# Performance work log

Measured on AMD Instinct MI355X. Metric: run time of the kernel, lower is better.

The kernel has to match this reference:

```python
import jax, jax.numpy as jnp
import numpy as np
import math

H, C = 16, 4


def _clustering(x, alv, mu, log_var, log_prior, mi_estimation):
    # x: [B,h,L,D], alv: [B,h,L], mu/log_var: [h or 1, C, D], log_prior: [h or 1, C]
    B, Hh, L, D = x.shape
    z = x  # eval mode: no reparameterization noise
    zd = z[:, :, :, None, :]                       # [B,h,L,1,D]
    mu_b = mu[:, None, :, :]                       # [h,1,C,D]
    lv = log_var[:, None, :, :]
    var = jnp.exp(lv)
    lp = jax.nn.log_softmax(log_prior, axis=-1)    # [h,C]
    mse = (zd - mu_b) ** 2 / var                   # [B,h,L,C,D]
    log_pdf = -0.5 * mse.sum(-1) - 0.5 * lv.sum(-1) - D * math.pi  # [B,h,L,C]
    log_pdf = log_pdf + lp[:, None, :]
    shift = jax.lax.stop_gradient(log_pdf.max(axis=-1, keepdims=True))
    log_probs = jax.nn.log_softmax(log_pdf - shift + 5.0, axis=-1)
    cp = jnp.exp(log_probs)                        # cluster probs [B,h,L,C]
    lp_b = jnp.broadcast_to(lp[None, :, None, :], log_probs.shape)
    # F.kl_div(log_probs, prior) = prior * (log prior - log_probs)
    kl = (jnp.exp(lp_b) * (lp_b - log_probs)).sum(-1).mean(axis=(1, 2))
    alv5 = alv[:, :, :, None, None]
    avar = jnp.exp(alv5)
    kl = kl + 0.5 * (cp * (mse + avar / var + lv).sum(-1)).sum(-1).mean(axis=(1, 2))
    kl = kl - 0.5 * ((1.0 + alv5).sum(-1) * D).mean(axis=(1, 2, 3))
    eye = jnp.eye(L, dtype=x.dtype)
    div = jnp.einsum('bhqc,bhkc->bhqk', cp, cp)
    div = ((div - eye) ** 2) * (eye * 1.25 + (1.0 - eye) * 0.75)
    div_loss = div.mean(axis=(1, 2, 3))
    if mi_estimation:
        pdf = jnp.exp(log_pdf - jax.lax.stop_gradient(log_pdf.max())).sum(-1, keepdims=True)
        w = cp * pdf
        mi_probs = w / jnp.maximum(w.sum(axis=2, keepdims=True), 1e-6)  # L1 normalize over L
        mi_p = jnp.minimum(jnp.einsum('bilc,bjlc->blij', mi_probs, cp), 1.0)
        mask_h = 1.0 - jnp.eye(Hh, dtype=x.dtype)
        mi_loss = -(jnp.log(1.0 - mi_p + 1e-6) * mask_h).mean(axis=(1, 2, 3)) * 10.0
        aff = jnp.einsum('bhqc,bhkc->bhqk', cp, cp)
        diag = jnp.diagonal(jax.nn.log_softmax(aff, axis=-1), axis1=2, axis2=3)
        mi_loss = mi_loss - diag.mean(axis=(1, 2))
    else:
        mi_loss = jnp.zeros_like(kl)
    return z, cp, kl, div_loss, mi_loss


def _forward(query, key, value, Wq, bq, Wk, bk, Wv, bv, Wo, bo, Wsem, bsem,
             Whead, bhead, tok_mu, tok_log_var, tok_log_prior,
             head_mu, head_log_var, head_log_prior):
    B, L, D = query.shape
    Dk = D // H
    q = query @ Wq + bq
    k = key @ Wk + bk
    v = value @ Wv + bv
    alv = (q @ Wsem + bsem).transpose(0, 2, 1)                 # [B,H,L]
    qh = q.reshape(B, L, H, Dk).transpose(0, 2, 1, 3)          # [B,H,L,Dk]
    z, cp_q, kl_q, div_q, _ = _clustering(qh, alv, tok_mu, tok_log_var, tok_log_prior, False)
    kh = k.reshape(B, L, H, Dk).transpose(0, 2, 1, 3)
    vh = v.reshape(B, L, H, Dk).transpose(0, 2, 1, 3)
    cluster_mask = jnp.einsum('bhqc,bhkc->bhqk', cp_q, cp_q)   # token-cluster affinity mask
    scores = jnp.einsum('bhqd,bhkd->bhqk', z, kh) / math.sqrt(Dk)
    attn = jax.nn.softmax(scores, axis=-1) * cluster_mask
    attn = attn / (attn.sum(axis=-1, keepdims=True) + 1e-6)
    ctx = jnp.einsum('bhqk,bhkd->bhqd', attn, vh)              # [B,H,L,Dk]
    ctx_f = ctx.transpose(0, 2, 1, 3).reshape(B, L, D)
    alv_h = (ctx_f @ Whead + bhead).transpose(0, 2, 1)         # [B,H,L]
    _, cp_h, kl_h, div_h, mi = _clustering(ctx, alv_h, head_mu, head_log_var, head_log_prior, True)
    out = ctx_f @ Wo + bo
    return out, attn.mean(axis=1), kl_q + kl_h, div_q + div_h, mi


def setup_inputs() -> dict:
    key = jax.random.key(0)
    ks = jax.random.split(key, 12)
    B, L, D = 8, 512, 1024
    Dk = D // H
    s = 1.0 / math.sqrt(D)
    f32 = jnp.float32
    inp = {
        'query': jax.random.normal(ks[0], (B, L, D), f32),
        'key': jax.random.normal(ks[1], (B, L, D), f32),
        'value': jax.random.normal(ks[2], (B, L, D), f32),
        'Wq': jax.random.normal(ks[3], (D, D), f32) * s, 'bq': jnp.zeros((D,), f32),
        'Wk': jax.random.normal(ks[4], (D, D), f32) * s, 'bk': jnp.zeros((D,), f32),
        'Wv': jax.random.normal(ks[5], (D, D), f32) * s, 'bv': jnp.zeros((D,), f32),
        'Wo': jax.random.normal(ks[6], (D, D), f32) * s, 'bo': jnp.zeros((D,), f32),
        'Wsem': jax.random.normal(ks[7], (D, H), f32) * s, 'bsem': jnp.zeros((H,), f32),
        'Whead': jax.random.normal(ks[8], (D, H), f32) * s, 'bhead': jnp.zeros((H,), f32),
        'tok_mu': jax.random.normal(ks[9], (H, C, Dk), f32) * 0.1,
        'tok_log_var': jnp.zeros((H, C, Dk), f32),
        'tok_log_prior': jnp.full((H, C), math.log(1.0 / C), f32),
        'head_mu': jax.random.normal(ks[10], (1, C, Dk), f32) * 0.1,
        'head_log_var': jnp.zeros((1, C, Dk), f32),
        'head_log_prior': jnp.full((1, C), math.log(1.0 / C), f32),
    }
    return inp


def reference(query, key, value, Wq, bq, Wk, bk, Wv, bv, Wo, bo, Wsem, bsem,
              Whead, bhead, tok_mu, tok_log_var, tok_log_prior,
              head_mu, head_log_var, head_log_prior):
    return _forward(query, key, value, Wq, bq, Wk, bk, Wv, bv, Wo, bo, Wsem, bsem,
                    Whead, bhead, tok_mu, tok_log_var, tok_log_prior,
                    head_mu, head_log_var, head_log_prior)
```

## Files before the change

### kernel.cpp

```cpp
#include <hip/hip_runtime.h>
#include <math.h>

#define BB 8
#define LL 512
#define DD 1024
#define HH 16
#define CC 4
#define DK 64
#define NEG_DPI 201.06192982974676f

typedef __attribute__((ext_vector_type(8))) short short8;
typedef __attribute__((ext_vector_type(4))) float floatx4;
typedef __attribute__((ext_vector_type(8))) unsigned short u16x8;
typedef __attribute__((ext_vector_type(4))) unsigned short u16x4;

__device__ inline float block_sum256(float v, float* s_red) {
    int t = threadIdx.x;
    s_red[t] = v; __syncthreads();
    for (int off = 128; off > 0; off >>= 1) {
        if (t < off) s_red[t] += s_red[t + off];
        __syncthreads();
    }
    float r = s_red[0]; __syncthreads();
    return r;
}
__device__ inline float block_max256(float v, float* s_red) {
    int t = threadIdx.x;
    s_red[t] = v; __syncthreads();
    for (int off = 128; off > 0; off >>= 1) {
        if (t < off) s_red[t] = fmaxf(s_red[t], s_red[t + off]);
        __syncthreads();
    }
    float r = s_red[0]; __syncthreads();
    return r;
}
__device__ inline unsigned int fenc(float f) {
    unsigned int b = __float_as_uint(f);
    return (b & 0x80000000u) ? ~b : (b | 0x80000000u);
}
__device__ inline float fdec(unsigned int u) {
    return (u & 0x80000000u) ? __uint_as_float(u ^ 0x80000000u) : __uint_as_float(~u);
}
__device__ inline unsigned short f2bf(float x) {
    unsigned int u = __float_as_uint(x);
    return (unsigned short)((u + 0x7FFFu + ((u >> 16) & 1u)) >> 16);
}
__device__ inline float bf2f(unsigned short h) {
    return __uint_as_float((unsigned int)h << 16);
}

__global__ __launch_bounds__(256)
void convert_hilo(const float* __restrict__ x, unsigned short* __restrict__ hh,
                  unsigned short* __restrict__ ll) {
    int i = blockIdx.x * 256 + threadIdx.x;
    float4 v = ((const float4*)x)[i];
    u16x4 h, l;
    float c[4] = {v.x, v.y, v.z, v.w};
#pragma unroll
    for (int j = 0; j < 4; j++) {
        unsigned short hb = f2bf(c[j]);
        h[j] = hb;
        l[j] = f2bf(c[j] - bf2f(hb));
    }
    ((u16x4*)hh)[i] = h;
    ((u16x4*)ll)[i] = l;
}

__global__ __launch_bounds__(256)
void wconv4(const float* __restrict__ W0, const float* __restrict__ W1,
            const float* __restrict__ W2, const float* __restrict__ W3,
            unsigned short* __restrict__ Tbase) {
    __shared__ float tile[64][65];
    int z = blockIdx.z;
    const float* W = (z == 0) ? W0 : (z == 1) ? W1 : (z == 2) ? W2 : W3;
    const size_t WS = (size_t)DD * DD;
    unsigned short* Th = Tbase + (size_t)z * 2 * WS;
    unsigned short* Tl = Th + WS;
    int t = threadIdx.x;
    int n0 = blockIdx.x * 64, k0 = blockIdx.y * 64;
    int r = t >> 4, c4 = (t & 15) * 4;
#pragma unroll
    for (int rr = 0; rr < 64; rr += 16) {
        float4 v = *(const float4*)&W[(size_t)(k0 + r + rr) * DD + n0 + c4];
        tile[r + rr][c4 + 0] = v.x; tile[r + rr][c4 + 1] = v.y;
        tile[r + rr][c4 + 2] = v.z; tile[r + rr][c4 + 3] = v.w;
    }
    __syncthreads();
    int rn = t >> 2, kg = (t & 3) * 16;
    u16x8 oh[2], ol[2];
#pragma unroll
    for (int j = 0; j < 16; j++) {
        float x = tile[kg + j][rn];
        unsigned short hb = f2bf(x);
        oh[j >> 3][j & 7] = hb;
        ol[j >> 3][j & 7] = f2bf(x - bf2f(hb));
    }
    size_t o = (size_t)(n0 + rn) * DD + k0 + kg;
    *(u16x8*)&Th[o] = oh[0]; *(u16x8*)&Th[o + 8] = oh[1];
    *(u16x8*)&Tl[o] = ol[0]; *(u16x8*)&Tl[o + 8] = ol[1];
}

__device__ __forceinline__
void gemm_body(const unsigned short* __restrict__ Ah, const unsigned short* __restrict__ Al,
               const unsigned short* __restrict__ Bh, const unsigned short* __restrict__ Bl,
               const float* __restrict__ bias, float* __restrict__ C,
               unsigned short* __restrict__ Ch, unsigned short* __restrict__ Cl) {
    __shared__ unsigned short sAh[128 * 32];
    __shared__ unsigned short sAl[128 * 32];
    __shared__ unsigned short sBh[128 * 32];
    __shared__ unsigned short sBl[128 * 32];
    int t = threadIdx.x;
    int n0 = blockIdx.x * 128, m0 = blockIdx.y * 128;
    int lane = t & 63, w = t >> 6;
    int wm = w >> 1, wn = w & 1;
    int lm = lane & 15, quad = lane >> 4;
    int srow = t >> 1, sk = (t & 1) * 16;

    const unsigned short* gAh = Ah + (size_t)(m0 + srow) * DD + sk;
    const unsigned short* gAl = Al + (size_t)(m0 + srow) * DD + sk;
    const unsigned short* gBh = Bh + (size_t)(n0 + srow) * DD + sk;
    const unsigned short* gBl = Bl + (size_t)(n0 + srow) * DD + sk;
    unsigned short* wAh = &sAh[srow * 32 + sk];
    unsigned short* wAl = &sAl[srow * 32 + sk];
    unsigned short* wBh = &sBh[srow * 32 + sk];
    unsigned short* wBl = &sBl[srow * 32 + sk];

    floatx4 acc[4][4] = {};

    for (int kt = 0; kt < 32; kt++) {
        int kb = kt * 32;
        u16x8 a0 = *(const u16x8*)(gAh + kb);
        u16x8 a1 = *(const u16x8*)(gAh + kb + 8);
        u16x8 a2 = *(const u16x8*)(gAl + kb);
        u16x8 a3 = *(const u16x8*)(gAl + kb + 8);
        u16x8 b0 = *(const u16x8*)(gBh + kb);
        u16x8 b1 = *(const u16x8*)(gBh + kb + 8);
        u16x8 b2 = *(const u16x8*)(gBl + kb);
        u16x8 b3 = *(const u16x8*)(gBl + kb + 8);
        __syncthreads();
        *(u16x8*)(wAh) = a0; *(u16x8*)(wAh + 8) = a1;
        *(u16x8*)(wAl) = a2; *(u16x8*)(wAl + 8) = a3;
        *(u16x8*)(wBh) = b0; *(u16x8*)(wBh + 8) = b1;
        *(u16x8*)(wBl) = b2; *(u16x8*)(wBl + 8) = b3;
        __syncthreads();

        short8 bh[4], bl[4];
#pragma unroll
        for (int j = 0; j < 4; j++) {
            int nb = (wn * 64 + j * 16 + lm) * 32 + quad * 8;
            bh[j] = *(const short8*)&sBh[nb];
            bl[j] = *(const short8*)&sBl[nb];
        }
#pragma unroll
        for (int i = 0; i < 4; i++) {
            int ab = (wm * 64 + i * 16 + lm) * 32 + quad * 8;
            short8 ah = *(const short8*)&sAh[ab];
            short8 al = *(const short8*)&sAl[ab];
#pragma unroll
            for (int j = 0; j < 4; j++) {
                acc[i][j] = __builtin_amdgcn_mfma_f32_16x16x32_bf16(ah, bh[j], acc[i][j], 0, 0, 0);
                acc[i][j] = __builtin_amdgcn_mfma_f32_16x16x32_bf16(ah, bl[j], acc[i][j], 0, 0, 0);
                acc[i][j] = __builtin_amdgcn_mfma_f32_16x16x32_bf16(al, bh[j], acc[i][j], 0, 0, 0);
            }
        }
    }
#pragma unroll
    for (int i = 0; i < 4; i++) {
#pragma unroll
        for (int j = 0; j < 4; j++) {
            int n = n0 + wn * 64 + j * 16 + lm;
            float bv = bias[n];
#pragma unroll
            for (int r = 0; r < 4; r++) {
                int m = m0 + wm * 64 + i * 16 + quad * 4 + r;
                size_t idx = (size_t)m * DD + n;
                float val = acc[i][j][r] + bv;
                if (C) C[idx] = val;
                if (Ch) {
                    unsigned short hb = f2bf(val);
                    Ch[idx] = hb;
                    Cl[idx] = f2bf(val - bf2f(hb));
                }
            }
        }
    }
}

__global__ __launch_bounds__(256)
void mfma_gemm_bias(const unsigned short* __restrict__ Ah, const unsigned short* __restrict__ Al,
                    const unsigned short* __restrict__ Bh, const unsigned short* __restrict__ Bl,
                    const float* __restrict__ bias, float* __restrict__ C,
                    unsigned short* __restrict__ Ch, unsigned short* __restrict__ Cl) {
    gemm_body(Ah, Al, Bh, Bl, bias, C, Ch, Cl);
}

__global__ __launch_bounds__(256)
void mfma_gemm_qkv(const unsigned short* __restrict__ ist3, const unsigned short* __restrict__ wbase,
                   const float* __restrict__ bq, const float* __restrict__ bk,
                   const float* __restrict__ bv, float* __restrict__ Cq,
                   unsigned short* __restrict__ obase) {
    int z = blockIdx.z;
    const size_t NB = (size_t)BB * LL * DD;
    const size_t WS = (size_t)DD * DD;
    const unsigned short* Ah = ist3 + (size_t)z * 2 * NB;
    const unsigned short* Bh = wbase + (size_t)z * 2 * WS;
    const float* bias = (z == 0) ? bq : (z == 1) ? bk : bv;
    float* C = (z == 0) ? Cq : nullptr;
    unsigned short* Ch = obase + (size_t)z * 2 * NB;
    gemm_body(Ah, Ah + NB, Bh, Bh + WS, bias, C, Ch, Ch + NB);
}

__global__ __launch_bounds__(256)
void vt_prep2(const unsigned short* __restrict__ voh, const unsigned short* __restrict__ vol,
              unsigned short* __restrict__ vth, unsigned short* __restrict__ vtl) {
    __shared__ unsigned short tile[128 * 68];
    int t = threadIdx.x;
    int which = blockIdx.x & 1;
    int l0 = (blockIdx.x >> 1) * 128, h = blockIdx.y, b = blockIdx.z;
    const unsigned short* src = which ? vol : voh;
    unsigned short* dst = which ? vtl : vth;
#pragma unroll
    for (int i = 0; i < 8; i++) {
        int u = t + i * 256;
        int l = u >> 4, c4 = (u & 15) * 4;
        u16x4 v4 = *(const u16x4*)&src[((size_t)(b * LL + l0 + l)) * DD + h * DK + c4];
        tile[l * 68 + c4 + 0] = v4[0]; tile[l * 68 + c4 + 1] = v4[1];
        tile[l * 68 + c4 + 2] = v4[2]; tile[l * 68 + c4 + 3] = v4[3];
    }
    __syncthreads();
    size_t ob = ((size_t)(b * HH + h)) * DK * LL;
#pragma unroll
    for (int i = 0; i < 8; i++) {
        int u = t + i * 256;
        int d = u >> 5, lq = (u & 31) * 4;
        u16x4 o;
#pragma unroll
        for (int j = 0; j < 4; j++) o[j] = tile[(lq + j) * 68 + d];
        *(u16x4*)&dst[ob + (size_t)d * LL + l0 + lq] = o;
    }
}

__global__ __launch_bounds__(256)
void alv_gemm(const float* __restrict__ A, const float* __restrict__ Wp,
              const float* __restrict__ bias, float* __restrict__ alv) {
    __shared__ float As[16][65];
    __shared__ float Ws[64][17];
    int t = threadIdx.x;
    int m0 = blockIdx.x * 16;
    int r = t >> 4, hh = t & 15;
    float acc = 0.f;
    for (int kt = 0; kt < 16; kt++) {
        __syncthreads();
#pragma unroll
        for (int i = 0; i < 4; i++) {
            int e = t + i * 256;
            int rr = e >> 6, kk = e & 63;
            As[rr][kk] = A[(size_t)(m0 + rr) * DD + kt * 64 + kk];
        }
#pragma unroll
        for (int i = 0; i < 4; i++) {
            int e = t + i * 256;
            int kk = e >> 4, h2 = e & 15;
            Ws[kk][h2] = Wp[(size_t)(kt * 64 + kk) * HH + h2];
        }
        __syncthreads();
#pragma unroll
        for (int kk = 0; kk < 64; kk++) acc += As[r][kk] * Ws[kk][hh];
    }
    int m = m0 + r;
    int b = m >> 9, l = m & 511;
    alv[(size_t)(b * HH + hh) * LL + l] = acc + bias[hh];
}

__global__ __launch_bounds__(256)
void cluster_kernel(const float* __restrict__ zsrc, const float* __restrict__ alv,
                    const float* __restrict__ mu, const float* __restrict__ logvar,
                    const float* __restrict__ logprior,
                    float* __restrict__ cp_out, float* __restrict__ lpdf_out,
                    unsigned int* __restrict__ maxenc, float* __restrict__ kl_out,
                    int isHead) {
    __shared__ float s_mu[CC * DK], s_iv[CC * DK], s_lv[CC * DK];
    __shared__ float s_slv[CC], s_siv[CC], s_lp[CC];
    __shared__ float s_red[256];
    int t = threadIdx.x;
    int tile = blockIdx.x & 1;
    int bh = blockIdx.x >> 1;
    int h = bh & (HH - 1), b = bh >> 4;
    int hm = isHead ? 0 : h;

    {
        float m = mu[hm * CC * DK + t];
        float lv = logvar[hm * CC * DK + t];
        s_mu[t] = m; s_lv[t] = lv; s_iv[t] = expf(-lv);
    }
    __syncthreads();
    if (t < CC) {
        float slv = 0.f, siv = 0.f;
        for (int d = 0; d < DK; d++) { slv += s_lv[t * DK + d]; siv += s_iv[t * DK + d]; }
        s_slv[t] = slv; s_siv[t] = siv;
    }
    if (t == CC) {
        float x[CC];
        float m = -1e30f;
        for (int c = 0; c < CC; c++) { x[c] = logprior[hm * CC + c]; m = fmaxf(m, x[c]); }
        float se = 0.f;
        for (int c = 0; c < CC; c++) se += expf(x[c] - m);
        float lse = m + logf(se);
        for (int c = 0; c < CC; c++) s_lp[c] = x[c] - lse;
    }
    __syncthreads();

    int l = tile * 256 + t;
    const float* zp = zsrc + ((size_t)(b * LL + l)) * DD + h * DK;
    float acc[CC] = {0.f, 0.f, 0.f, 0.f};
    for (int d = 0; d < DK; d += 4) {
        float4 z4 = *(const float4*)(zp + d);
#pragma unroll
        for (int c = 0; c < CC; c++) {
            float d0 = z4.x - s_mu[c * DK + d];     acc[c] += d0 * d0 * s_iv[c * DK + d];
            float d1 = z4.y - s_mu[c * DK + d + 1]; acc[c] += d1 * d1 * s_iv[c * DK + d + 1];
            float d2 = z4.z - s_mu[c * DK + d + 2]; acc[c] += d2 * d2 * s_iv[c * DK + d + 2];
            float d3 = z4.w - s_mu[c * DK + d + 3]; acc[c] += d3 * d3 * s_iv[c * DK + d + 3];
        }
    }
    float lpdf[CC];
#pragma unroll
    for (int c = 0; c < CC; c++)
        lpdf[c] = -0.5f * acc[c] - 0.5f * s_slv[c] - NEG_DPI + s_lp[c];
    float m = fmaxf(fmaxf(lpdf[0], lpdf[1]), fmaxf(lpdf[2], lpdf[3]));
    float se = 0.f;
#pragma unroll
    for (int c = 0; c < CC; c++) se += expf(lpdf[c] - m);
    float lse = m + logf(se);
    float lprob[CC], cpv[CC];
    size_t idx = ((size_t)(bh * LL + l)) * CC;
#pragma unroll
    for (int c = 0; c < CC; c++) {
        lprob[c] = lpdf[c] - lse;
        cpv[c] = expf(lprob[c]);
        cp_out[idx + c] = cpv[c];
    }
    if (isHead) {
#pragma unroll
        for (int c = 0; c < CC; c++) lpdf_out[idx + c] = lpdf[c];
    }
    float alvv = alv[(size_t)bh * LL + l];
    float avar = expf(alvv);
    float t1 = 0.f, t2 = 0.f;
#pragma unroll
    for (int c = 0; c < CC; c++) {
        t1 += expf(s_lp[c]) * (s_lp[c] - lprob[c]);
        t2 += cpv[c] * (acc[c] + avar * s_siv[c] + s_slv[c]);
    }
    float klv = t1 + 0.5f * t2 - 0.5f * (float)DK * (1.0f + alvv);
    float tot = block_sum256(klv, s_red);
    if (t == 0) atomicAdd(kl_out + b, tot * (1.0f / (HH * LL)));
    if (isHead) {
        float mt = block_max256(m, s_red);
        if (t == 0) atomicMax(maxenc, fenc(mt));
    }
}

__global__ __launch_bounds__(256)
void pairstats_kernel(const float* __restrict__ cp, float* __restrict__ div_out,
                      float* __restrict__ mi_out, int isHead) {
    __shared__ float s_cp[LL * CC];
    __shared__ float s_red[256];
    int t = threadIdx.x;
    int bh = blockIdx.x >> 3;
    int seg = blockIdx.x & 7;
    int b = bh >> 4;
    const float* base = cp + (size_t)bh * LL * CC;
#pragma unroll
    for (int i = 0; i < 2; i++) {
        int e = t + i * 256;
        *(float4*)&s_cp[e * 4] = *(const float4*)&base[e * 4];
    }
    __syncthreads();

    int q = seg * 64 + (t >> 2);
    int ln = t & 3;
    float4 cq = *(float4*)&s_cp[q * 4];
    float divacc = 0.f, m = -1e30f, s = 0.f, selfdot = 0.f;
    for (int k = ln; k < LL; k += 4) {
        float4 ck = *(float4*)&s_cp[k * 4];
        float dot = cq.x * ck.x + cq.y * ck.y + cq.z * ck.z + cq.w * ck.w;
        float del = (k == q) ? 1.f : 0.f;
        float dd = dot - del;
        divacc += dd * dd * (0.75f + 0.5f * del);
        if (isHead) {
            if (dot > m) { s = s * expf(m - dot) + 1.f; m = dot; }
            else         { s += expf(dot - m); }
            if (k == q) selfdot = dot;
        }
    }
#pragma unroll
    for (int off = 1; off <= 2; off <<= 1) divacc += __shfl_xor(divacc, off, 64);
    float diag = 0.f;
    if (isHead) {
#pragma unroll
        for (int off = 1; off <= 2; off <<= 1) {
            float om = __shfl_xor(m, off, 64);
            float os = __shfl_xor(s, off, 64);
            float nm = fmaxf(m, om);
            s = s * expf(m - nm) + os * expf(om - nm);
            m = nm;
        }
#pragma unroll
        for (int off = 1; off <= 2; off <<= 1) selfdot += __shfl_xor(selfdot, off, 64);
        diag = selfdot - (m + logf(s));
    }
    float dtot = block_sum256(ln == 0 ? divacc : 0.f, s_red);
    if (t == 0) atomicAdd(div_out + b, dtot * (1.0f / ((float)HH * LL * LL)));
    if (isHead) {
        float gtot = block_sum256(ln == 0 ? diag : 0.f, s_red);
        if (t == 0) atomicAdd(mi_out + b, -gtot * (1.0f / (HH * LL)));
    }
}

__global__ __launch_bounds__(256)
void attn4_kernel(const unsigned short* __restrict__ qoh, const unsigned short* __restrict__ qol,
                  const unsigned short* __restrict__ koh, const unsigned short* __restrict__ kol,
                  const unsigned short* __restrict__ vth, const unsigned short* __restrict__ vtl,
                  const float* __restrict__ cpq,
                  float* __restrict__ ctxf, float* __restrict__ attn_out) {
    __shared__ __align__(16) char sbuf[34048];
    __shared__ float s_inv[16];
    float* S = (float*)sbuf;
    unsigned short* Ph = (unsigned short*)sbuf;
    unsigned short* Pl = Ph + 16 * 520;

    int t = threadIdx.x;
    int id = blockIdx.x;
    int xcd = id & 7;
    int s = id >> 3;
    int qt = s & 31;
    int combo = ((s >> 5) << 3) | xcd;
    int hg = combo & 3;
    int b = combo >> 2;
    int q0 = qt * 16;
    int lane = t & 63, w = t >> 6;
    int lm = lane & 15, quad = lane >> 4;

    float4 pm[8] = {};

#pragma unroll 1
    for (int hi = 0; hi < 4; hi++) {
        int h = hg * 4 + hi;
        int bh = b * HH + h;

        size_t qbase = ((size_t)(b * LL + q0 + lm)) * DD + h * DK + quad * 8;
        short8 qah0 = *(const short8*)(qoh + qbase);
        short8 qah1 = *(const short8*)(qoh + qbase + 32);
        short8 qal0 = *(const short8*)(qol + qbase);
        short8 qal1 = *(const short8*)(qol + qbase + 32);

        floatx4 sa[8] = {};
#pragma unroll
        for (int j = 0; j < 8; j++) {
            int n0 = w * 128 + j * 16;
            size_t kbase = ((size_t)(b * LL + n0 + lm)) * DD + h * DK + quad * 8;
            short8 kbh0 = *(const short8*)(koh + kbase);
            short8 kbh1 = *(const short8*)(koh + kbase + 32);
            short8 kbl0 = *(const short8*)(kol + kbase);
            short8 kbl1 = *(const short8*)(kol + kbase + 32);
            sa[j] = __builtin_amdgcn_mfma_f32_16x16x32_bf16(qah0, kbh0, sa[j], 0, 0, 0);
            sa[j] = __builtin_amdgcn_mfma_f32_16x16x32_bf16(qah1, kbh1, sa[j], 0, 0, 0);
            sa[j] = __builtin_amdgcn_mfma_f32_16x16x32_bf16(qah0, kbl0, sa[j], 0, 0, 0);
            sa[j] = __builtin_amdgcn_mfma_f32_16x16x32_bf16(qah1, kbl1, sa[j], 0, 0, 0);
            sa[j] = __builtin_amdgcn_mfma_f32_16x16x32_bf16(qal0, kbh0, sa[j], 0, 0, 0);
            sa[j] = __builtin_amdgcn_mfma_f32_16x16x32_bf16(qal1, kbh1, sa[j], 0, 0, 0);
        }
        __syncthreads();
#pragma unroll
        for (int j = 0; j < 8; j++) {
            int kc = w * 128 + j * 16 + lm;
#pragma unroll
            for (int r = 0; r < 4; r++)
                S[(quad * 4 + r) * 532 + kc] = sa[j][r] * 0.125f;
        }
        __syncthreads();

        {
            int r = t >> 4, ln = t & 15;
            const float4* cpb = (const float4*)(cpq + (size_t)bh * LL * CC);
            float m = -1e30f;
            for (int k = ln; k < LL; k += 16) m = fmaxf(m, S[r * 532 + k]);
#pragma unroll
            for (int off = 8; off > 0; off >>= 1) m = fmaxf(m, __shfl_xor(m, off, 16));
            float4 cq = cpb[q0 + r];
            float Z = 0.f, Sm = 0.f;
            for (int k = ln; k < LL; k += 16) {
                float e = expf(S[r * 532 + k] - m);
                float4 ck = cpb[k];
                float mask = cq.x * ck.x + cq.y * ck.y + cq.z * ck.z + cq.w * ck.w;
                float a = e * mask;
                Z += e; Sm += a;
                S[r * 532 + k] = a;
            }
#pragma unroll
            for (int off = 8; off > 0; off >>= 1) {
                Z += __shfl_xor(Z, off, 16);
                Sm += __shfl_xor(Sm, off, 16);
            }
            if (ln == 0) s_inv[r] = 1.f / (Sm + 1e-6f * Z);
        }
        __syncthreads();

        float4 pv[8];
#pragma unroll
        for (int i = 0; i < 8; i++) {
            int e = t + i * 256;
            int r2 = e >> 7, k4 = (e & 127) * 4;
            float4 p = *(float4*)&S[r2 * 532 + k4];
            float inv = s_inv[r2];
            p.x *= inv; p.y *= inv; p.z *= inv; p.w *= inv;
            pm[i].x += p.x; pm[i].y += p.y; pm[i].z += p.z; pm[i].w += p.w;
            pv[i] = p;
        }
        __syncthreads();
#pragma unroll
        for (int i = 0; i < 8; i++) {
            int e = t + i * 256;
            int r2 = e >> 7, k4 = (e & 127) * 4;
            float c[4] = {pv[i].x, pv[i].y, pv[i].z, pv[i].w};
            u16x4 hv, lv;
#pragma unroll
            for (int j = 0; j < 4; j++) {
                unsigned short hb = f2bf(c[j]);
                hv[j] = hb;
                lv[j] = f2bf(c[j] - bf2f(hb));
            }
            *(u16x4*)&Ph[r2 * 520 + k4] = hv;
            *(u16x4*)&Pl[r2 * 520 + k4] = lv;
        }
        __syncthreads();

        int dn = w * 16 + lm;
        const unsigned short* vrh = vth + ((size_t)bh * DK + dn) * LL;
        const unsigned short* vrl = vtl + ((size_t)bh * DK + dn) * LL;
        floatx4 ca = {};
#pragma unroll
        for (int kc = 0; kc < 16; kc++) {
            int kb = kc * 32 + quad * 8;
            short8 pah = *(const short8*)&Ph[lm * 520 + kb];
            short8 pal = *(const short8*)&Pl[lm * 520 + kb];
            short8 vbh = *(const short8*)(vrh + kb);
            short8 vbl = *(const short8*)(vrl + kb);
            ca = __builtin_amdgcn_mfma_f32_16x16x32_bf16(pah, vbh, ca, 0, 0, 0);
            ca = __builtin_amdgcn_mfma_f32_16x16x32_bf16(pah, vbl, ca, 0, 0, 0);
            ca = __builtin_amdgcn_mfma_f32_16x16x32_bf16(pal, vbh, ca, 0, 0, 0);
        }
#pragma unroll
        for (int r = 0; r < 4; r++)
            ctxf[((size_t)(b * LL + q0 + quad * 4 + r)) * DD + h * DK + dn] = ca[r];
    }

    const float sc = 1.0f / (float)HH;
#pragma unroll
    for (int i = 0; i < 8; i++) {
        int e = t + i * 256;
        int r2 = e >> 7, k4 = (e & 127) * 4;
        float* dst = attn_out + ((size_t)(b * LL + q0 + r2)) * LL + k4;
        unsafeAtomicAdd(dst + 0, pm[i].x * sc);
        unsafeAtomicAdd(dst + 1, pm[i].y * sc);
        unsafeAtomicAdd(dst + 2, pm[i].z * sc);
        unsafeAtomicAdd(dst + 3, pm[i].w * sc);
    }
}

__global__ __launch_bounds__(256)
void wsum_kernel(const float* __restrict__ lpdf, const float* __restrict__ cp,
                 const unsigned int* __restrict__ maxenc,
                 float* __restrict__ pdf_out, float* __restrict__ wsum_out) {
    __shared__ float s_red[256];
    int t = threadIdx.x;
    int bh = blockIdx.x;
    float M = fdec(*maxenc);
    float a[CC] = {0.f, 0.f, 0.f, 0.f};
    for (int li = 0; li < 2; li++) {
        int l = t + li * 256;
        size_t idx = ((size_t)bh * LL + l) * CC;
        float p0 = expf(lpdf[idx + 0] - M);
        float p1 = expf(lpdf[idx + 1] - M);
        float p2 = expf(lpdf[idx + 2] - M);
        float p3 = expf(lpdf[idx + 3] - M);
        float pd = p0 + p1 + p2 + p3;
        pdf_out[(size_t)bh * LL + l] = pd;
        a[0] += cp[idx + 0] * pd; a[1] += cp[idx + 1] * pd;
        a[2] += cp[idx + 2] * pd; a[3] += cp[idx + 3] * pd;
    }
#pragma unroll
    for (int c = 0; c < CC; c++) {
        float tot = block_sum256(a[c], s_red);
        if (t == 0) wsum_out[bh * CC + c] = tot;
    }
}

__global__ __launch_bounds__(256)
void mi_kernel(const float* __restrict__ cp, const float* __restrict__ pdf,
               const float* __restrict__ wsum, float* __restrict__ mi_out) {
    __shared__ float s_q[HH * CC];
    __shared__ float s_c[HH * CC];
    __shared__ float s_red[256];
    int t = threadIdx.x;
    int b = blockIdx.x >> 9;
    int l = blockIdx.x & 511;
    if (t < HH * CC) {
        int i = t >> 2, c = t & 3;
        float cpv = cp[((size_t)(b * HH + i) * LL + l) * CC + c];
        s_c[t] = cpv;
        float w = cpv * pdf[(size_t)(b * HH + i) * LL + l];
        float ws = wsum[(b * HH + i) * CC + c];
        s_q[t] = w / fmaxf(ws, 1e-6f);
    }
    __syncthreads();
    int i = t >> 4, j = t & 15;
    float sdot = 0.f;
#pragma unroll
    for (int c = 0; c < CC; c++) sdot += s_q[i * 4 + c] * s_c[j * 4 + c];
    float mi_p = fminf(sdot, 1.f);
    float val = (i != j) ? logf(1.f - mi_p + 1e-6f) : 0.f;
    float tot = block_sum256(val, s_red);
    if (t == 0) atomicAdd(mi_out + b, -10.f * tot * (1.0f / ((float)LL * HH * HH)));
}

extern "C" void kernel_launch(void* const* d_in, const int* in_sizes, int n_in,
                              void* d_out, int out_size, void* d_ws, size_t ws_size,
                              hipStream_t stream) {
    (void)in_sizes; (void)n_in; (void)out_size; (void)ws_size;
    const float* query  = (const float*)d_in[0];
    const float* key    = (const float*)d_in[1];
    const float* value  = (const float*)d_in[2];
    const float* Wq     = (const float*)d_in[3];
    const float* bq     = (const float*)d_in[4];
    const float* Wk     = (const float*)d_in[5];
    const float* bk     = (const float*)d_in[6];
    const float* Wv     = (const float*)d_in[7];
    const float* bv     = (const float*)d_in[8];
    const float* Wo     = (const float*)d_in[9];
    const float* bo     = (const float*)d_in[10];
    const float* Wsem   = (const float*)d_in[11];
    const float* bsem   = (const float*)d_in[12];
    const float* Whead  = (const float*)d_in[13];
    const float* bhead  = (const float*)d_in[14];
    const float* tokmu  = (const float*)d_in[15];
    const float* toklv  = (const float*)d_in[16];
    const float* toklp  = (const float*)d_in[17];
    const float* headmu = (const float*)d_in[18];
    const float* headlv = (const float*)d_in[19];
    const float* headlp = (const float*)d_in[20];

    float* ws   = (float*)d_ws;
    const size_t NBLD = (size_t)BB * LL * DD;
    float* q    = ws;
    float* ctxf = ws + NBLD;
    float* alvq = ws + 2 * NBLD;
    float* alvh = alvq + (size_t)BB * HH * LL;
    float* cpq  = alvh + (size_t)BB * HH * LL;
    float* cph  = cpq + (size_t)BB * HH * LL * CC;
    float* lpdfh= cph + (size_t)BB * HH * LL * CC;
    float* pdfb = lpdfh + (size_t)BB * HH * LL * CC;
    float* wsumb= pdfb + (size_t)BB * HH * LL;
    unsigned int* maxenc = (unsigned int*)(wsumb + (size_t)BB * HH * CC);
    float* scr3 = (float*)(maxenc + 4);

    unsigned short* us = (unsigned short*)(scr3 + (size_t)BB * 8 * LL * LL);
    const size_t WSZ = (size_t)DD * DD;
    unsigned short* ist_h = us;
    unsigned short* ist_l = ist_h + NBLD;
    unsigned short* qoh = ist_l + NBLD;
    unsigned short* qol = qoh + NBLD;
    unsigned short* koh = qol + NBLD;
    unsigned short* kol = koh + NBLD;
    unsigned short* voh = kol + NBLD;
    unsigned short* vol = voh + NBLD;
    unsigned short* vth = vol + NBLD;
    unsigned short* vtl = vth + NBLD;
    unsigned short* wqh = vtl + NBLD;
    unsigned short* wql = wqh + WSZ;
    unsigned short* wkh = wql + WSZ;
    unsigned short* wkl = wkh + WSZ;
    unsigned short* wvh = wkl + WSZ;
    unsigned short* wvl = wvh + WSZ;
    unsigned short* woh = wvl + WSZ;
    unsigned short* wol = woh + WSZ;

    unsigned short* ist3 = (unsigned short*)scr3;

    float* out      = (float*)d_out;
    float* attn_out = out + NBLD;
    float* kl_out   = attn_out + (size_t)BB * LL * LL;
    float* div_out  = kl_out + BB;
    float* mi_out   = div_out + BB;

    hipMemsetAsync(kl_out, 0, 3 * BB * sizeof(float), stream);
    hipMemsetAsync(maxenc, 0, sizeof(unsigned int), stream);
    hipMemsetAsync(attn_out, 0, (size_t)BB * LL * LL * sizeof(float), stream);

    wconv4<<<dim3(16, 16, 4), 256, 0, stream>>>(Wq, Wk, Wv, Wo, wqh);

    convert_hilo<<<NBLD / 1024, 256, 0, stream>>>(query, ist3,            ist3 + NBLD);
    convert_hilo<<<NBLD / 1024, 256, 0, stream>>>(key,   ist3 + 2 * NBLD, ist3 + 3 * NBLD);
    convert_hilo<<<NBLD / 1024, 256, 0, stream>>>(value, ist3 + 4 * NBLD, ist3 + 5 * NBLD);
    mfma_gemm_qkv<<<dim3(DD / 128, BB * LL / 128, 3), 256, 0, stream>>>(
        ist3, wqh, bq, bk, bv, q, qoh);

    vt_prep2<<<dim3(2 * LL / 128, HH, BB), 256, 0, stream>>>(voh, vol, vth, vtl);

    alv_gemm<<<BB * LL / 16, 256, 0, stream>>>(q, Wsem, bsem, alvq);
    cluster_kernel<<<BB * HH * 2, 256, 0, stream>>>(q, alvq, tokmu, toklv, toklp,
                                                    cpq, nullptr, nullptr, kl_out, 0);
    pairstats_kernel<<<BB * HH * 8, 256, 0, stream>>>(cpq, div_out, nullptr, 0);

    attn4_kernel<<<dim3(1024), 256, 0, stream>>>(
        qoh, qol, koh, kol, vth, vtl, cpq, ctxf, attn_out);

    convert_hilo<<<NBLD / 1024, 256, 0, stream>>>(ctxf, ist_h, ist_l);
    alv_gemm<<<BB * LL / 16, 256, 0, stream>>>(ctxf, Whead, bhead, alvh);
    cluster_kernel<<<BB * HH * 2, 256, 0, stream>>>(ctxf, alvh, headmu, headlv, headlp,
                                                    cph, lpdfh, maxenc, kl_out, 1);
    pairstats_kernel<<<BB * HH * 8, 256, 0, stream>>>(cph, div_out, mi_out, 1);
    wsum_kernel<<<BB * HH, 256, 0, stream>>>(lpdfh, cph, maxenc, pdfb, wsumb);
    mi_kernel<<<BB * LL, 256, 0, stream>>>(cph, pdfb, wsumb, mi_out);
    mfma_gemm_bias<<<dim3(DD / 128, BB * LL / 128), 256, 0, stream>>>(
        ist_h, ist_l, woh, wol, bo, out, nullptr, nullptr);
}
```

Before: 880.8 us.

## Split attention per head into two launches with scratch buffer reduction instead of atomics

Result: faster. 795.7 us (-9.7%).

```diff
diff --git a/kernel.cpp b/kernel.cpp
--- a/kernel.cpp
+++ b/kernel.cpp
@@ -419,12 +419,14 @@
 }
 
 __global__ __launch_bounds__(256)
-void attn4_kernel(const unsigned short* __restrict__ qoh, const unsigned short* __restrict__ qol,
+void attn3_kernel(const unsigned short* __restrict__ qoh, const unsigned short* __restrict__ qol,
                   const unsigned short* __restrict__ koh, const unsigned short* __restrict__ kol,
                   const unsigned short* __restrict__ vth, const unsigned short* __restrict__ vtl,
                   const float* __restrict__ cpq,
-                  float* __restrict__ ctxf, float* __restrict__ attn_out) {
-    __shared__ __align__(16) char sbuf[34048];
+                  float* __restrict__ ctxf, unsigned short* __restrict__ cxh,
+                  unsigned short* __restrict__ cxl,
+                  float* __restrict__ attn_h, int h0) {
+    __shared__ __align__(16) char sbuf[33280];
     __shared__ float s_inv[16];
     float* S = (float*)sbuf;
     unsigned short* Ph = (unsigned short*)sbuf;
@@ -433,140 +435,147 @@
     int t = threadIdx.x;
     int id = blockIdx.x;
     int xcd = id & 7;
-    int s = id >> 3;
-    int qt = s & 31;
-    int combo = ((s >> 5) << 3) | xcd;
-    int hg = combo & 3;
-    int b = combo >> 2;
+    int sid = id >> 3;
+    int qt = sid & 31;
+    int combo = ((sid >> 5) << 3) | xcd;
+    int hl = combo & 7;
+    int b = combo >> 3;
+    int h = h0 + hl;
     int q0 = qt * 16;
     int lane = t & 63, w = t >> 6;
     int lm = lane & 15, quad = lane >> 4;
-
-    float4 pm[8] = {};
-
-#pragma unroll 1
-    for (int hi = 0; hi < 4; hi++) {
-        int h = hg * 4 + hi;
-        int bh = b * HH + h;
-
-        size_t qbase = ((size_t)(b * LL + q0 + lm)) * DD + h * DK + quad * 8;
-        short8 qah0 = *(const short8*)(qoh + qbase);
-        short8 qah1 = *(const short8*)(qoh + qbase + 32);
-        short8 qal0 = *(const short8*)(qol + qbase);
-        short8 qal1 = *(const short8*)(qol + qbase + 32);
-
-        floatx4 sa[8] = {};
-#pragma unroll
-        for (int j = 0; j < 8; j++) {
-            int n0 = w * 128 + j * 16;
-            size_t kbase = ((size_t)(b * LL + n0 + lm)) * DD + h * DK + quad * 8;
-            short8 kbh0 = *(const short8*)(koh + kbase);
-            short8 kbh1 = *(const short8*)(koh + kbase + 32);
-            short8 kbl0 = *(const short8*)(kol + kbase);
-            short8 kbl1 = *(const short8*)(kol + kbase + 32);
-            sa[j] = __builtin_amdgcn_mfma_f32_16x16x32_bf16(qah0, kbh0, sa[j], 0, 0, 0);
-            sa[j] = __builtin_amdgcn_mfma_f32_16x16x32_bf16(qah1, kbh1, sa[j], 0, 0, 0);
-            sa[j] = __builtin_amdgcn_mfma_f32_16x16x32_bf16(qah0, kbl0, sa[j], 0, 0, 0);
-            sa[j] = __builtin_amdgcn_mfma_f32_16x16x32_bf16(qah1, kbl1, sa[j], 0, 0, 0);
-            sa[j] = __builtin_amdgcn_mfma_f32_16x16x32_bf16(qal0, kbh0, sa[j], 0, 0, 0);
-            sa[j] = __builtin_amdgcn_mfma_f32_16x16x32_bf16(qal1, kbh1, sa[j], 0, 0, 0);
-        }
-        __syncthreads();
-#pragma unroll
-        for (int j = 0; j < 8; j++) {
-            int kc = w * 128 + j * 16 + lm;
-#pragma unroll
-            for (int r = 0; r < 4; r++)
-                S[(quad * 4 + r) * 532 + kc] = sa[j][r] * 0.125f;
-        }
-        __syncthreads();
-
-        {
-            int r = t >> 4, ln = t & 15;
-            const float4* cpb = (const float4*)(cpq + (size_t)bh * LL * CC);
-            float m = -1e30f;
-            for (int k = ln; k < LL; k += 16) m = fmaxf(m, S[r * 532 + k]);
-#pragma unroll
-            for (int off = 8; off > 0; off >>= 1) m = fmaxf(m, __shfl_xor(m, off, 16));
-            float4 cq = cpb[q0 + r];
-            float Z = 0.f, Sm = 0.f;
-            for (int k = ln; k < LL; k += 16) {
-                float e = expf(S[r * 532 + k] - m);
-                float4 ck = cpb[k];
-                float mask = cq.x * ck.x + cq.y * ck.y + cq.z * ck.z + cq.w * ck.w;
-                float a = e * mask;
-                Z += e; Sm += a;
-                S[r * 532 + k] = a;
-            }
-#pragma unroll
-            for (int off = 8; off > 0; off >>= 1) {
-                Z += __shfl_xor(Z, off, 16);
-                Sm += __shfl_xor(Sm, off, 16);
-            }
-            if (ln == 0) s_inv[r] = 1.f / (Sm + 1e-6f * Z);
-        }
-        __syncthreads();
-
-        float4 pv[8];
-#pragma unroll
-        for (int i = 0; i < 8; i++) {
-            int e = t + i * 256;
-            int r2 = e >> 7, k4 = (e & 127) * 4;
-            float4 p = *(float4*)&S[r2 * 532 + k4];
-            float inv = s_inv[r2];
-            p.x *= inv; p.y *= inv; p.z *= inv; p.w *= inv;
-            pm[i].x += p.x; pm[i].y += p.y; pm[i].z += p.z; pm[i].w += p.w;
-            pv[i] = p;
-        }
-        __syncthreads();
-#pragma unroll
-        for (int i = 0; i < 8; i++) {
-            int e = t + i * 256;
-            int r2 = e >> 7, k4 = (e & 127) * 4;
-            float c[4] = {pv[i].x, pv[i].y, pv[i].z, pv[i].w};
-            u16x4 hv, lv;
-#pragma unroll
-            for (int j = 0; j < 4; j++) {
-                unsigned short hb = f2bf(c[j]);
-                hv[j] = hb;
-                lv[j] = f2bf(c[j] - bf2f(hb));
-            }
-            *(u16x4*)&Ph[r2 * 520 + k4] = hv;
-            *(u16x4*)&Pl[r2 * 520 + k4] = lv;
-        }
-        __syncthreads();
-
-        int dn = w * 16 + lm;
-        const unsigned short* vrh = vth + ((size_t)bh * DK + dn) * LL;
-        const unsigned short* vrl = vtl + ((size_t)bh * DK + dn) * LL;
-        floatx4 ca = {};
-#pragma unroll
-        for (int kc = 0; kc < 16; kc++) {
-            int kb = kc * 32 + quad * 8;
-            short8 pah = *(const short8*)&Ph[lm * 520 + kb];
-            short8 pal = *(const short8*)&Pl[lm * 520 + kb];
-            short8 vbh = *(const short8*)(vrh + kb);
-            short8 vbl = *(const short8*)(vrl + kb);
-            ca = __builtin_amdgcn_mfma_f32_16x16x32_bf16(pah, vbh, ca, 0, 0, 0);
-            ca = __builtin_amdgcn_mfma_f32_16x16x32_bf16(pah, vbl, ca, 0, 0, 0);
-            ca = __builtin_amdgcn_mfma_f32_16x16x32_bf16(pal, vbh, ca, 0, 0, 0);
-        }
+    int bh = b * HH + h;
+
+    size_t qbase = ((size_t)(b * LL + q0 + lm)) * DD + h * DK + quad * 8;
+    short8 qah0 = *(const short8*)(qoh + qbase);
+    short8 qah1 = *(const short8*)(qoh + qbase + 32);
+    short8 qal0 = *(const short8*)(qol + qbase);
+    short8 qal1 = *(const short8*)(qol + qbase + 32);
+
+    floatx4 sa[8] = {};
+#pragma unroll
+    for (int j = 0; j < 8; j++) {
+        int n0 = w * 128 + j * 16;
+        size_t kbase = ((size_t)(b * LL + n0 + lm)) * DD + h * DK + quad * 8;
+        short8 kbh0 = *(const short8*)(koh + kbase);
+        short8 kbh1 = *(const short8*)(koh + kbase + 32);
+        short8 kbl0 = *(const short8*)(kol + kbase);
+        short8 kbl1 = *(const short8*)(kol + kbase + 32);
+        sa[j] = __builtin_amdgcn_mfma_f32_16x16x32_bf16(qah0, kbh0, sa[j], 0, 0, 0);
+        sa[j] = __builtin_amdgcn_mfma_f32_16x16x32_bf16(qah1, kbh1, sa[j], 0, 0, 0);
+        sa[j] = __builtin_amdgcn_mfma_f32_16x16x32_bf16(qah0, kbl0, sa[j], 0, 0, 0);
+        sa[j] = __builtin_amdgcn_mfma_f32_16x16x32_bf16(qah1, kbl1, sa[j], 0, 0, 0);
+        sa[j] = __builtin_amdgcn_mfma_f32_16x16x32_bf16(qal0, kbh0, sa[j], 0, 0, 0);
+        sa[j] = __builtin_amdgcn_mfma_f32_16x16x32_bf16(qal1, kbh1, sa[j], 0, 0, 0);
+    }
+#pragma unroll
+    for (int j = 0; j < 8; j++) {
+        int kc = w * 128 + j * 16 + lm;
 #pragma unroll
         for (int r = 0; r < 4; r++)
-            ctxf[((size_t)(b * LL + q0 + quad * 4 + r)) * DD + h * DK + dn] = ca[r];
-    }
-
-    const float sc = 1.0f / (float)HH;
+            S[(quad * 4 + r) * 516 + kc] = sa[j][r] * 0.125f;
+    }
+    __syncthreads();
+
+    {
+        int r = t >> 4, ln = t & 15;
+        const float4* cpb = (const float4*)(cpq + (size_t)bh * LL * CC);
+        float m = -1e30f;
+        for (int k = ln; k < LL; k += 16) m = fmaxf(m, S[r * 516 + k]);
+#pragma unroll
+        for (int off = 8; off > 0; off >>= 1) m = fmaxf(m, __shfl_xor(m, off, 16));
+        float4 cq = cpb[q0 + r];
+        float Z = 0.f, Sm = 0.f;
+        for (int k = ln; k < LL; k += 16) {
+            float e = expf(S[r * 516 + k] - m);
+            float4 ck = cpb[k];
+            float mask = cq.x * ck.x + cq.y * ck.y + cq.z * ck.z + cq.w * ck.w;
+            float a = e * mask;
+            Z += e; Sm += a;
+            S[r * 516 + k] = a;
+        }
+#pragma unroll
+        for (int off = 8; off > 0; off >>= 1) {
+            Z += __shfl_xor(Z, off, 16);
+            Sm += __shfl_xor(Sm, off, 16);
+        }
+        if (ln == 0) s_inv[r] = 1.f / (Sm + 1e-6f * Z);
+    }
+    __syncthreads();
+
+    float4 pv[8];
 #pragma unroll
     for (int i = 0; i < 8; i++) {
         int e = t + i * 256;
         int r2 = e >> 7, k4 = (e & 127) * 4;
-        float* dst = attn_out + ((size_t)(b * LL + q0 + r2)) * LL + k4;
-        unsafeAtomicAdd(dst + 0, pm[i].x * sc);
-        unsafeAtomicAdd(dst + 1, pm[i].y * sc);
-        unsafeAtomicAdd(dst + 2, pm[i].z * sc);
-        unsafeAtomicAdd(dst + 3, pm[i].w * sc);
-    }
+        float4 p = *(float4*)&S[r2 * 516 + k4];
+        float inv = s_inv[r2];
+        p.x *= inv; p.y *= inv; p.z *= inv; p.w *= inv;
+        pv[i] = p;
+        *(float4*)&attn_h[(((size_t)((b * 8 + hl) * LL + q0 + r2)) * LL) + k4] = p;
+    }
+    __syncthreads();
+#pragma unroll
+    for (int i = 0; i < 8; i++) {
+        int e = t + i * 256;
+        int r2 = e >> 7, k4 = (e & 127) * 4;
+        float c[4] = {pv[i].x, pv[i].y, pv[i].z, pv[i].w};
+        u16x4 hv, lv;
+#pragma unroll
+        for (int j = 0; j < 4; j++) {
+            unsigned short hb = f2bf(c[j]);
+            hv[j] = hb;
+            lv[j] = f2bf(c[j] - bf2f(hb));
+        }
+        *(u16x4*)&Ph[r2 * 520 + k4] = hv;
+        *(u16x4*)&Pl[r2 * 520 + k4] = lv;
+    }
+    __syncthreads();
+
+    int dn = w * 16 + lm;
+    const unsigned short* vrh = vth + ((size_t)bh * DK + dn) * LL;
+    const unsigned short* vrl = vtl + ((size_t)bh * DK + dn) * LL;
+    floatx4 ca = {};
+#pragma unroll
+    for (int kc = 0; kc < 16; kc++) {
+        int kb = kc * 32 + quad * 8;
+        short8 pah = *(const short8*)&Ph[lm * 520 + kb];
+        short8 pal = *(const short8*)&Pl[lm * 520 + kb];
+        short8 vbh = *(const short8*)(vrh + kb);
+        short8 vbl = *(const short8*)(vrl + kb);
+        ca = __builtin_amdgcn_mfma_f32_16x16x32_bf16(pah, vbh, ca, 0, 0, 0);
+        ca = __builtin_amdgcn_mfma_f32_16x16x32_bf16(pah, vbl, ca, 0, 0, 0);
+        ca = __builtin_amdgcn_mfma_f32_16x16x32_bf16(pal, vbh, ca, 0, 0, 0);
+    }
+#pragma unroll
+    for (int r = 0; r < 4; r++) {
+        float val = ca[r];
+        size_t idx = ((size_t)(b * LL + q0 + quad * 4 + r)) * DD + h * DK + dn;
+        ctxf[idx] = val;
+        unsigned short hb = f2bf(val);
+        cxh[idx] = hb;
+        cxl[idx] = f2bf(val - bf2f(hb));
+    }
+}
+
+__global__ __launch_bounds__(256)
+void attn_reduce(const float* __restrict__ attn_h, float* __restrict__ attn_out,
+                 int accumulate) {
+    int e = blockIdx.x * 256 + threadIdx.x;
+    int b = e >> 16;
+    int rem = e & 65535;
+    float4 s = {0.f, 0.f, 0.f, 0.f};
+#pragma unroll
+    for (int hl = 0; hl < 8; hl++) {
+        float4 v = ((const float4*)attn_h)[(((size_t)(b * 8 + hl)) << 16) + rem];
+        s.x += v.x; s.y += v.y; s.z += v.z; s.w += v.w;
+    }
+    float4* o = (float4*)attn_out + (((size_t)b) << 16) + rem;
+    const float sc = 1.0f / (float)HH;
+    float4 prev = {0.f, 0.f, 0.f, 0.f};
+    if (accumulate) prev = *o;
+    prev.x += s.x * sc; prev.y += s.y * sc; prev.z += s.z * sc; prev.w += s.w * sc;
+    *o = prev;
 }
 
 __global__ __launch_bounds__(256)
@@ -687,6 +696,7 @@
     unsigned short* wol = woh + WSZ;
 
     unsigned short* ist3 = (unsigned short*)scr3;
+    float* attn_h = scr3;
 
     float* out      = (float*)d_out;
     float* attn_out = out + NBLD;
@@ -696,7 +706,6 @@
 
     hipMemsetAsync(kl_out, 0, 3 * BB * sizeof(float), stream);
     hipMemsetAsync(maxenc, 0, sizeof(unsigned int), stream);
-    hipMemsetAsync(attn_out, 0, (size_t)BB * LL * LL * sizeof(float), stream);
 
     wconv4<<<dim3(16, 16, 4), 256, 0, stream>>>(Wq, Wk, Wv, Wo, wqh);
 
@@ -713,10 +722,13 @@
                                                     cpq, nullptr, nullptr, kl_out, 0);
     pairstats_kernel<<<BB * HH * 8, 256, 0, stream>>>(cpq, div_out, nullptr, 0);
 
-    attn4_kernel<<<dim3(1024), 256, 0, stream>>>(
-        qoh, qol, koh, kol, vth, vtl, cpq, ctxf, attn_out);
-
-    convert_hilo<<<NBLD / 1024, 256, 0, stream>>>(ctxf, ist_h, ist_l);
+    for (int h0 = 0; h0 < HH; h0 += 8) {
+        attn3_kernel<<<dim3(2048), 256, 0, stream>>>(
+            qoh, qol, koh, kol, vth, vtl, cpq, ctxf, ist_h, ist_l, attn_h, h0);
+        attn_reduce<<<BB * LL * LL / 4 / 256, 256, 0, stream>>>(
+            attn_h, attn_out, h0 > 0 ? 1 : 0);
+    }
+
     alv_gemm<<<BB * LL / 16, 256, 0, stream>>>(ctxf, Whead, bhead, alvh);
     cluster_kernel<<<BB * HH * 2, 256, 0, stream>>>(ctxf, alvh, headmu, headlv, headlp,
                                                     cph, lpdfh, maxenc, kl_out, 1);
```
